# Optimization experiments

Measured on AMD Instinct MI355X. Metric: run time of the kernel, lower is better.

Reference implementation:

```python
import jax, jax.numpy as jnp
import numpy as np

MAX_VALUE = 127.0  # signed 8-bit: 2**(8-1)-1


def _quantize_int8(t, amax):
    # per-tensor symmetric quantization: round(x * 127/amax), clamped to [-127, 127]
    scale = MAX_VALUE / amax
    return jnp.clip(jnp.round(t * scale), -MAX_VALUE, MAX_VALUE).astype(jnp.int8)


def setup_inputs() -> dict:
    key = jax.random.key(0)
    k1, k2, k3 = jax.random.split(key, 3)
    N, K, M = 8192, 4096, 4096
    x = jax.random.normal(k1, (N, K), dtype=jnp.float32)
    weight = jax.random.normal(k2, (M, K), dtype=jnp.float32) * (1.0 / np.sqrt(K))
    bias = jax.random.normal(k3, (M,), dtype=jnp.float32) * (1.0 / np.sqrt(K))
    return {"x": x, "weight": weight, "bias": bias}


def reference(x, weight, bias):
    # amax from max-abs calibration (per-tensor), as TensorQuantizer would hold
    amax = jnp.max(jnp.abs(x))
    amax_w = jnp.max(jnp.abs(weight))
    qi = _quantize_int8(x, amax)          # [N, K] int8
    qw = _quantize_int8(weight, amax_w)   # [M, K] int8
    acc = jnp.matmul(qi.astype(jnp.int32), qw.astype(jnp.int32).T)  # [N, M] int32
    # dequant: output / ((max/amax) * (max/amax_w)), then bias
    dequant = (amax * amax_w) / (MAX_VALUE * MAX_VALUE)
    return acc.astype(jnp.float32) * dequant + bias
```

## Files before the change

### kernel.cpp

```cpp
#include <hip/hip_runtime.h>

#define K_DIM 4096
#define N_DIM 8192
#define M_DIM 4096

typedef int v4i __attribute__((ext_vector_type(4)));

__global__ void amax2_kernel(const float4* __restrict__ x,
                             const float4* __restrict__ w,
                             unsigned* __restrict__ scal) {
  const int XB = 2048, WB = 1024;
  const float4* p;
  int n4, b, nb;
  unsigned* out;
  if (blockIdx.x < XB) {
    p = x; n4 = N_DIM * K_DIM / 4; out = scal + 0; b = blockIdx.x; nb = XB;
  } else {
    p = w; n4 = M_DIM * K_DIM / 4; out = scal + 1; b = blockIdx.x - XB; nb = WB;
  }
  int tid = b * blockDim.x + threadIdx.x;
  int stride = nb * blockDim.x;
  float m = 0.f;
  for (int i = tid; i < n4; i += stride) {
    float4 v = p[i];
    m = fmaxf(m, fmaxf(fmaxf(fabsf(v.x), fabsf(v.y)),
                       fmaxf(fabsf(v.z), fabsf(v.w))));
  }
#pragma unroll
  for (int off = 32; off > 0; off >>= 1)
    m = fmaxf(m, __shfl_down(m, off));
  __shared__ float sm[4];
  int lane = threadIdx.x & 63, wv = threadIdx.x >> 6;
  if (lane == 0) sm[wv] = m;
  __syncthreads();
  if (threadIdx.x == 0) {
    m = fmaxf(fmaxf(sm[0], sm[1]), fmaxf(sm[2], sm[3]));
    atomicMax(out, __float_as_uint(m));
  }
}

__device__ __forceinline__ unsigned pack4(float4 v, float s) {
  int q0 = (int)fminf(fmaxf(rintf(v.x * s), -127.f), 127.f);
  int q1 = (int)fminf(fmaxf(rintf(v.y * s), -127.f), 127.f);
  int q2 = (int)fminf(fmaxf(rintf(v.z * s), -127.f), 127.f);
  int q3 = (int)fminf(fmaxf(rintf(v.w * s), -127.f), 127.f);
  return (unsigned)(q0 & 255) | ((unsigned)(q1 & 255) << 8) |
         ((unsigned)(q2 & 255) << 16) | ((unsigned)(q3 & 255) << 24);
}

__global__ void quant2_kernel(const float4* __restrict__ x,
                              const float4* __restrict__ w,
                              int4* __restrict__ qx, int4* __restrict__ qw,
                              const unsigned* __restrict__ scal) {
  const int XB = 2048, WB = 1024;
  const float4* in;
  int4* out;
  int n16, b, nb;
  float amax;
  if (blockIdx.x < XB) {
    in = x; out = qx; n16 = N_DIM * K_DIM / 16; b = blockIdx.x; nb = XB;
    amax = __uint_as_float(scal[0]);
  } else {
    in = w; out = qw; n16 = M_DIM * K_DIM / 16; b = blockIdx.x - XB; nb = WB;
    amax = __uint_as_float(scal[1]);
  }
  float s = 127.0f / amax;
  int tid = b * blockDim.x + threadIdx.x;
  int stride = nb * blockDim.x;
  for (int i = tid; i < n16; i += stride) {
    float4 v0 = in[4 * i + 0];
    float4 v1 = in[4 * i + 1];
    float4 v2 = in[4 * i + 2];
    float4 v3 = in[4 * i + 3];
    int4 o;
    o.x = (int)pack4(v0, s);
    o.y = (int)pack4(v1, s);
    o.z = (int)pack4(v2, s);
    o.w = (int)pack4(v3, s);
    out[i] = o;
  }
}

__device__ __forceinline__ void gld_lds16(const void* g, void* l) {
  __builtin_amdgcn_global_load_lds(
      (const __attribute__((address_space(1))) void*)g,
      (__attribute__((address_space(3))) void*)l, 16, 0, 0);
}

__global__ __launch_bounds__(256, 2) void gemm_i8(
    const signed char* __restrict__ A,
    const signed char* __restrict__ B,
    const float* __restrict__ bias,
    float* __restrict__ out,
    const unsigned* __restrict__ scal)
{
  __shared__ signed char la[128 * 128];
  __shared__ signed char lb[128 * 128];

  const int tid = threadIdx.x;
  const int lane = tid & 63;
  const int w = tid >> 6;
  const int wr = (w & 1) * 64;
  const int wc = (w >> 1) * 64;
  const long r0 = (long)blockIdx.x * 128;
  const long c0 = (long)blockIdx.y * 128;

  const int srow = tid >> 3;
  const int gcol = ((tid & 7) ^ (srow & 7)) * 16;
  const signed char* ga = A + (r0 + srow) * K_DIM + gcol;
  const signed char* gb = B + (c0 + srow) * K_DIM + gcol;

  v4i acc[4][4];
#pragma unroll
  for (int i = 0; i < 4; ++i)
#pragma unroll
    for (int j = 0; j < 4; ++j) acc[i][j] = (v4i){0, 0, 0, 0};

  const int fr = lane & 15;
  const int fq = lane >> 4;
  const int sa = fr & 7;

  for (int k0 = 0; k0 < K_DIM; k0 += 128) {
#pragma unroll
    for (int p = 0; p < 4; ++p) {
      gld_lds16(ga + (long)p * 32 * K_DIM + k0, la + p * 4096 + tid * 16);
      gld_lds16(gb + (long)p * 32 * K_DIM + k0, lb + p * 4096 + tid * 16);
    }
    __syncthreads();

#pragma unroll
    for (int ks = 0; ks < 2; ++ks) {
      v4i av[4], bv[4];
#pragma unroll
      for (int i = 0; i < 4; ++i)
        av[i] = *(const v4i*)(la + (wr + i * 16 + fr) * 128 +
                              (((ks * 4 + fq) ^ sa) * 16));
#pragma unroll
      for (int j = 0; j < 4; ++j)
        bv[j] = *(const v4i*)(lb + (wc + j * 16 + fr) * 128 +
                              (((ks * 4 + fq) ^ sa) * 16));
#pragma unroll
      for (int i = 0; i < 4; ++i)
#pragma unroll
        for (int j = 0; j < 4; ++j)
          acc[i][j] = __builtin_amdgcn_mfma_i32_16x16x64_i8(av[i], bv[j],
                                                            acc[i][j], 0, 0, 0);
    }
    __syncthreads();
  }

  const float dq =
      (__uint_as_float(scal[0]) * __uint_as_float(scal[1])) / 16129.0f;
  float bs[4];
#pragma unroll
  for (int j = 0; j < 4; ++j) bs[j] = bias[c0 + wc + j * 16 + fr];

#pragma unroll
  for (int i = 0; i < 4; ++i) {
    const long rbase = r0 + wr + i * 16 + fq * 4;
#pragma unroll
    for (int j = 0; j < 4; ++j) {
      const long c = c0 + wc + j * 16 + fr;
#pragma unroll
      for (int t = 0; t < 4; ++t) {
        out[(rbase + t) * (long)M_DIM + c] = (float)acc[i][j][t] * dq + bs[j];
      }
    }
  }
}

extern "C" void kernel_launch(void* const* d_in, const int* in_sizes, int n_in,
                              void* d_out, int out_size, void* d_ws, size_t ws_size,
                              hipStream_t stream) {
  const float* x = (const float*)d_in[0];
  const float* wt = (const float*)d_in[1];
  const float* bias = (const float*)d_in[2];
  float* out = (float*)d_out;

  unsigned* scal = (unsigned*)d_ws;
  signed char* qx = (signed char*)d_ws + 256;
  signed char* qw = qx + (long)N_DIM * K_DIM;

  hipMemsetAsync(d_ws, 0, 16, stream);

  amax2_kernel<<<3072, 256, 0, stream>>>((const float4*)x, (const float4*)wt,
                                         scal);
  quant2_kernel<<<3072, 256, 0, stream>>>((const float4*)x, (const float4*)wt,
                                          (int4*)qx, (int4*)qw, scal);

  dim3 grid(N_DIM / 128, M_DIM / 128);
  gemm_i8<<<grid, 256, 0, stream>>>(qx, qw, bias, out, scal);
}
```

Baseline: 443.2 us.

## Enlarge GEMM tile to 256x256 with double-buffered LDS prefetch

The int8 GEMM moves from 128x128 tiles with 4 waves to 256x256 tiles with 8 waves. It double-buffers LDS so the async global-to-LDS loads for k-tile t+2 overlap compute on tile t, with explicit vmcnt waits and barriers, and raises wave priority around MFMA bursts. This aims to cut global traffic per FLOP and hide load latency. The quant kernel is also simplified to one float4 per thread iteration. The cost is 128KB of LDS per block, which may allow only one block per CU, plus more accumulator registers.

```diff
diff --git a/kernel.cpp b/kernel.cpp
--- a/kernel.cpp
+++ b/kernel.cpp
@@ -50,35 +50,24 @@
 
 __global__ void quant2_kernel(const float4* __restrict__ x,
                               const float4* __restrict__ w,
-                              int4* __restrict__ qx, int4* __restrict__ qw,
+                              unsigned* __restrict__ qx, unsigned* __restrict__ qw,
                               const unsigned* __restrict__ scal) {
   const int XB = 2048, WB = 1024;
   const float4* in;
-  int4* out;
-  int n16, b, nb;
+  unsigned* out;
+  int n4, b, nb;
   float amax;
   if (blockIdx.x < XB) {
-    in = x; out = qx; n16 = N_DIM * K_DIM / 16; b = blockIdx.x; nb = XB;
+    in = x; out = qx; n4 = N_DIM * K_DIM / 4; b = blockIdx.x; nb = XB;
     amax = __uint_as_float(scal[0]);
   } else {
-    in = w; out = qw; n16 = M_DIM * K_DIM / 16; b = blockIdx.x - XB; nb = WB;
+    in = w; out = qw; n4 = M_DIM * K_DIM / 4; b = blockIdx.x - XB; nb = WB;
     amax = __uint_as_float(scal[1]);
   }
   float s = 127.0f / amax;
   int tid = b * blockDim.x + threadIdx.x;
   int stride = nb * blockDim.x;
-  for (int i = tid; i < n16; i += stride) {
-    float4 v0 = in[4 * i + 0];
-    float4 v1 = in[4 * i + 1];
-    float4 v2 = in[4 * i + 2];
-    float4 v3 = in[4 * i + 3];
-    int4 o;
-    o.x = (int)pack4(v0, s);
-    o.y = (int)pack4(v1, s);
-    o.z = (int)pack4(v2, s);
-    o.w = (int)pack4(v3, s);
-    out[i] = o;
-  }
+  for (int i = tid; i < n4; i += stride) out[i] = pack4(in[i], s);
 }
 
 __device__ __forceinline__ void gld_lds16(const void* g, void* l) {
@@ -87,32 +76,32 @@
       (__attribute__((address_space(3))) void*)l, 16, 0, 0);
 }
 
-__global__ __launch_bounds__(256, 2) void gemm_i8(
+__global__ __launch_bounds__(512, 2) void gemm_i8(
     const signed char* __restrict__ A,
     const signed char* __restrict__ B,
     const float* __restrict__ bias,
     float* __restrict__ out,
     const unsigned* __restrict__ scal)
 {
-  __shared__ signed char la[128 * 128];
-  __shared__ signed char lb[128 * 128];
+  __shared__ signed char lds[2][2][256 * 128];
 
   const int tid = threadIdx.x;
   const int lane = tid & 63;
   const int w = tid >> 6;
-  const int wr = (w & 1) * 64;
-  const int wc = (w >> 1) * 64;
-  const long r0 = (long)blockIdx.x * 128;
-  const long c0 = (long)blockIdx.y * 128;
+  const int wm = w >> 2;
+  const int wn = w & 3;
+  const long r0 = (long)blockIdx.x * 256;
+  const long c0 = (long)blockIdx.y * 256;
 
   const int srow = tid >> 3;
   const int gcol = ((tid & 7) ^ (srow & 7)) * 16;
   const signed char* ga = A + (r0 + srow) * K_DIM + gcol;
   const signed char* gb = B + (c0 + srow) * K_DIM + gcol;
-
-  v4i acc[4][4];
-#pragma unroll
-  for (int i = 0; i < 4; ++i)
+  const int ldst = tid * 16;
+
+  v4i acc[8][4];
+#pragma unroll
+  for (int i = 0; i < 8; ++i)
 #pragma unroll
     for (int j = 0; j < 4; ++j) acc[i][j] = (v4i){0, 0, 0, 0};
 
@@ -120,50 +109,76 @@
   const int fq = lane >> 4;
   const int sa = fr & 7;
 
-  for (int k0 = 0; k0 < K_DIM; k0 += 128) {
-#pragma unroll
-    for (int p = 0; p < 4; ++p) {
-      gld_lds16(ga + (long)p * 32 * K_DIM + k0, la + p * 4096 + tid * 16);
-      gld_lds16(gb + (long)p * 32 * K_DIM + k0, lb + p * 4096 + tid * 16);
+  auto STAGE = [&](int t, int buf) {
+    const long ko = (long)t * 128;
+    signed char* la = &lds[buf][0][0];
+    signed char* lb = &lds[buf][1][0];
+#pragma unroll
+    for (int p = 0; p < 4; ++p)
+      gld_lds16(ga + (long)p * 64 * K_DIM + ko, la + p * 8192 + ldst);
+#pragma unroll
+    for (int p = 0; p < 4; ++p)
+      gld_lds16(gb + (long)p * 64 * K_DIM + ko, lb + p * 8192 + ldst);
+  };
+
+  auto COMPUTE = [&](int buf) {
+    const signed char* la = &lds[buf][0][0];
+    const signed char* lb = &lds[buf][1][0];
+#pragma unroll
+    for (int ks = 0; ks < 2; ++ks) {
+      const int co = ((ks * 4 + fq) ^ sa) * 16;
+      v4i bv[4];
+#pragma unroll
+      for (int nf = 0; nf < 4; ++nf)
+        bv[nf] = *(const v4i*)(lb + (wn * 64 + nf * 16 + fr) * 128 + co);
+#pragma unroll
+      for (int mh = 0; mh < 2; ++mh) {
+        v4i av[4];
+#pragma unroll
+        for (int mi = 0; mi < 4; ++mi)
+          av[mi] =
+              *(const v4i*)(la + (wm * 128 + mh * 64 + mi * 16 + fr) * 128 + co);
+        __builtin_amdgcn_s_setprio(1);
+#pragma unroll
+        for (int mi = 0; mi < 4; ++mi)
+#pragma unroll
+          for (int nf = 0; nf < 4; ++nf)
+            acc[mh * 4 + mi][nf] = __builtin_amdgcn_mfma_i32_16x16x64_i8(
+                av[mi], bv[nf], acc[mh * 4 + mi][nf], 0, 0, 0);
+        __builtin_amdgcn_s_setprio(0);
+      }
     }
-    __syncthreads();
-
-#pragma unroll
-    for (int ks = 0; ks < 2; ++ks) {
-      v4i av[4], bv[4];
-#pragma unroll
-      for (int i = 0; i < 4; ++i)
-        av[i] = *(const v4i*)(la + (wr + i * 16 + fr) * 128 +
-                              (((ks * 4 + fq) ^ sa) * 16));
-#pragma unroll
-      for (int j = 0; j < 4; ++j)
-        bv[j] = *(const v4i*)(lb + (wc + j * 16 + fr) * 128 +
-                              (((ks * 4 + fq) ^ sa) * 16));
-#pragma unroll
-      for (int i = 0; i < 4; ++i)
-#pragma unroll
-        for (int j = 0; j < 4; ++j)
-          acc[i][j] = __builtin_amdgcn_mfma_i32_16x16x64_i8(av[i], bv[j],
-                                                            acc[i][j], 0, 0, 0);
-    }
-    __syncthreads();
-  }
+  };
+
+  const int NT = K_DIM / 128;
+  STAGE(0, 0);
+  STAGE(1, 1);
+  for (int t = 0; t < NT - 1; ++t) {
+    asm volatile("s_waitcnt vmcnt(8)" ::: "memory");
+    __builtin_amdgcn_s_barrier();
+    COMPUTE(t & 1);
+    __builtin_amdgcn_s_barrier();
+    if (t + 2 < NT) STAGE(t + 2, t & 1);
+  }
+  asm volatile("s_waitcnt vmcnt(0)" ::: "memory");
+  __builtin_amdgcn_s_barrier();
+  COMPUTE((NT - 1) & 1);
 
   const float dq =
       (__uint_as_float(scal[0]) * __uint_as_float(scal[1])) / 16129.0f;
   float bs[4];
 #pragma unroll
-  for (int j = 0; j < 4; ++j) bs[j] = bias[c0 + wc + j * 16 + fr];
-
-#pragma unroll
-  for (int i = 0; i < 4; ++i) {
-    const long rbase = r0 + wr + i * 16 + fq * 4;
-#pragma unroll
-    for (int j = 0; j < 4; ++j) {
-      const long c = c0 + wc + j * 16 + fr;
+  for (int nf = 0; nf < 4; ++nf) bs[nf] = bias[c0 + wn * 64 + nf * 16 + fr];
+
+#pragma unroll
+  for (int mf = 0; mf < 8; ++mf) {
+    const long rbase = r0 + wm * 128 + mf * 16 + fq * 4;
+#pragma unroll
+    for (int nf = 0; nf < 4; ++nf) {
+      const long c = c0 + wn * 64 + nf * 16 + fr;
 #pragma unroll
       for (int t = 0; t < 4; ++t) {
-        out[(rbase + t) * (long)M_DIM + c] = (float)acc[i][j][t] * dq + bs[j];
+        out[(rbase + t) * (long)M_DIM + c] = (float)acc[mf][nf][t] * dq + bs[nf];
       }
     }
   }
@@ -186,8 +201,8 @@
   amax2_kernel<<<3072, 256, 0, stream>>>((const float4*)x, (const float4*)wt,
                                          scal);
   quant2_kernel<<<3072, 256, 0, stream>>>((const float4*)x, (const float4*)wt,
-                                          (int4*)qx, (int4*)qw, scal);
-
-  dim3 grid(N_DIM / 128, M_DIM / 128);
-  gemm_i8<<<grid, 256, 0, stream>>>(qx, qw, bias, out, scal);
-}
+                                          (unsigned*)qx, (unsigned*)qw, scal);
+
+  dim3 grid(N_DIM / 256, M_DIM / 256);
+  gemm_i8<<<grid, 512, 0, stream>>>(qx, qw, bias, out, scal);
+}
```

Result: faster. 434.0 us (-2.1%).
